# Performance work log

Measured on AMD Instinct MI355X. Metric: run time of the kernel, lower is better.

## Reference

```python
import jax, jax.numpy as jnp
import numpy as np

K = 512       # knowledge_n = node count AND feature dim
S = 50000     # student_n
E_N = 6       # exer_n (hardcoded as literal 6 in the original forward)
DEG_K = 4     # exercise neighbors per knowledge node
DEG_S = 3     # exercise neighbors per student
NEG_SLOPE = 0.2  # PyG GATConv default


def setup_inputs() -> dict:
    key = jax.random.key(0)
    ks = jax.random.split(key, 10)
    kn_emb = jax.random.normal(ks[0], (K, K), jnp.float32)
    exer_emb = jax.random.normal(ks[1], (E_N, K), jnp.float32)
    all_stu_emb = jax.random.normal(ks[2], (S, K), jnp.float32)
    # k_from_e graph: nodes = [exercises(0..5), knowledge(6..6+K-1)]
    src_ke = jax.random.randint(ks[3], (K * DEG_K,), 0, E_N)
    dst_ke = E_N + jnp.repeat(jnp.arange(K), DEG_K)
    edges_ke = jnp.stack([src_ke, dst_ke]).astype(jnp.int32)   # e -> k
    edges_ek = edges_ke[::-1]                                  # k -> e
    # u_from_e graph: nodes = [exercises(0..5), students(6..6+S-1)]
    src_ue = jax.random.randint(ks[4], (S * DEG_S,), 0, E_N)
    dst_ue = E_N + jnp.repeat(jnp.arange(S), DEG_S)
    edges_ue = jnp.stack([src_ue, dst_ue]).astype(jnp.int32)   # e -> u
    edges_eu = edges_ue[::-1]                                  # u -> e
    sc = 1.0 / np.sqrt(K)
    W_gat = jax.random.normal(ks[5], (4, K, K), jnp.float32) * sc
    a_src = jax.random.normal(ks[6], (4, K), jnp.float32) * sc
    a_dst = jax.random.normal(ks[7], (4, K), jnp.float32) * sc
    b_gat = jnp.zeros((4, K), jnp.float32)
    attn_w = jax.random.normal(ks[8], (3, 2 * K), jnp.float32) / np.sqrt(2 * K)
    attn_b = jnp.zeros((3,), jnp.float32)
    return dict(kn_emb=kn_emb, exer_emb=exer_emb, all_stu_emb=all_stu_emb,
                W_gat=W_gat, a_src=a_src, a_dst=a_dst, b_gat=b_gat,
                attn_w=attn_w, attn_b=attn_b,
                edges_ke=edges_ke, edges_ek=edges_ek,
                edges_ue=edges_ue, edges_eu=edges_eu)


def _gat(x, edges, W, a_s, a_d, b, n):
    """Single-head PyG GATConv with self-loops. edges[0]=src, edges[1]=dst."""
    h = x @ W                                   # [n, K]
    loop = jnp.arange(n, dtype=edges.dtype)
    src = jnp.concatenate([edges[0], loop])
    dst = jnp.concatenate([edges[1], loop])
    alpha_s = h @ a_s                           # [n]
    alpha_d = h @ a_d
    e = jax.nn.leaky_relu(alpha_s[src] + alpha_d[dst], NEG_SLOPE)
    emax = jax.lax.stop_gradient(jax.ops.segment_max(e, dst, num_segments=n))
    ex = jnp.exp(e - emax[dst])
    den = jax.ops.segment_sum(ex, dst, num_segments=n)
    alpha = ex / den[dst]                       # per-dst softmax
    out = jax.ops.segment_sum(alpha[:, None] * h[src], dst, num_segments=n)
    return out + b


def reference(kn_emb, exer_emb, all_stu_emb, W_gat, a_src, a_dst, b_gat,
              attn_w, attn_b, edges_ke, edges_ek, edges_ue, edges_eu):
    e_k = jnp.concatenate([exer_emb, kn_emb], axis=0)        # [6+K, K]
    e_u = jnp.concatenate([exer_emb, all_stu_emb], axis=0)   # [6+S, K]
    n_ek, n_eu = e_k.shape[0], e_u.shape[0]
    k_from_e = _gat(e_k, edges_ke, W_gat[0], a_src[0], a_dst[0], b_gat[0], n_ek)
    e_from_k = _gat(e_k, edges_ek, W_gat[1], a_src[1], a_dst[1], b_gat[1], n_ek)
    u_from_e = _gat(e_u, edges_ue, W_gat[2], a_src[2], a_dst[2], b_gat[2], n_eu)
    e_from_u = _gat(e_u, edges_eu, W_gat[3], a_src[3], a_dst[3], b_gat[3], n_eu)
    # knowledge fusion (softmax over a single column -> all ones, kept faithful)
    D = k_from_e[E_N:]
    s3 = jnp.concatenate([kn_emb, D], axis=1) @ attn_w[0] + attn_b[0]   # [K]
    sc = jax.nn.softmax(s3[:, None], axis=1)
    kn_out = kn_emb + sc[:, 0:1] * D
    # exercise fusion: 2-way attention over knowledge/student messages
    B = e_from_k[:E_N]
    C = e_from_u[:E_N]
    s1 = jnp.concatenate([exer_emb, B], axis=1) @ attn_w[1] + attn_b[1]
    s2 = jnp.concatenate([exer_emb, C], axis=1) @ attn_w[2] + attn_b[2]
    sc2 = jax.nn.softmax(jnp.stack([s1, s2], axis=1), axis=1)           # [6, 2]
    exer_out = exer_emb + sc2[:, 0:1] * B + sc2[:, 1:2] * C
    stu_out = all_stu_emb + u_from_e[E_N:]
    return (kn_out, exer_out, stu_out)
```

## Files before the change

### kernel.cpp

```cpp
#include <hip/hip_runtime.h>

typedef __attribute__((ext_vector_type(4))) float f4;
typedef __attribute__((ext_vector_type(8))) short s8;

__device__ __forceinline__ unsigned short f2bf(float x){
  unsigned u = __float_as_uint(x);
  u += 0x7fffu + ((u >> 16) & 1u);
  return (unsigned short)(u >> 16);
}
__device__ __forceinline__ float lrelu(float v){ return v > 0.f ? v : 0.2f * v; }
__device__ __forceinline__ void gload16(const unsigned short* g, unsigned short* l){
  __builtin_amdgcn_global_load_lds((const __attribute__((address_space(1))) unsigned int*)g,
                                   (__attribute__((address_space(3))) unsigned int*)l, 16, 0, 0);
}

__global__ __launch_bounds__(256) void prep(const float* __restrict__ Wg,
    const float* __restrict__ a_src, const float* __restrict__ a_dst,
    const float* __restrict__ exer, float* __restrict__ pq, float* __restrict__ zbase,
    unsigned short* __restrict__ W2T, unsigned short* __restrict__ W0T,
    float* __restrict__ HE2, float* __restrict__ HE0)
{
  __shared__ float tile[32][33];
  __shared__ float xs[512];
  const int b = blockIdx.x, t = threadIdx.x;
  if (b < 512){
    const int m = b >> 8, kb = (b & 15) * 32, nb = ((b >> 4) & 15) * 32;
    const float* W = Wg + (m == 0 ? 2 * 262144 : 0);
    unsigned short* WT = (m == 0) ? W2T : W0T;
    const int tx = t & 31, ty = t >> 5;
    #pragma unroll
    for (int i = 0; i < 32; i += 8) tile[ty + i][tx] = W[(kb + ty + i) * 512 + nb + tx];
    __syncthreads();
    #pragma unroll
    for (int i = 0; i < 32; i += 8) WT[(nb + ty + i) * 512 + kb + tx] = f2bf(tile[tx][ty + i]);
  } else if (b < 768){
    const int tid = (b - 512) * 256 + t;
    if (tid < 12304) zbase[tid] = 0.f;
    const int wid = tid >> 6, lane = tid & 63;
    for (int task = wid; task < 4096; task += 1024){
      int g = task >> 10, isq = (task >> 9) & 1, r = task & 511;
      const float* w = Wg + ((g * 512 + r) << 9);
      const float* a = (isq ? a_dst : a_src) + g * 512;
      float s = 0.f;
      for (int i = lane; i < 512; i += 64) s += w[i] * a[i];
      for (int off = 32; off; off >>= 1) s += __shfl_down(s, off);
      if (lane == 0) pq[task] = s;
    }
  } else {
    const int b3 = b - 768;
    const int g = (b3 < 6) ? 0 : 2, e = b3 % 6;
    xs[t] = exer[e * 512 + t]; xs[t + 256] = exer[e * 512 + 256 + t];
    __syncthreads();
    const float* W = Wg + g * 262144;
    float a0 = 0.f, a1 = 0.f;
    #pragma unroll 8
    for (int k = 0; k < 512; k++){ float xv = xs[k]; a0 += xv * W[k * 512 + t]; a1 += xv * W[k * 512 + 256 + t]; }
    float* HE = (g == 0) ? HE0 : HE2;
    HE[e * 512 + t] = a0; HE[e * 512 + 256 + t] = a1;
  }
}

template<int DEG>
__device__ void pass1_body(float* sC, float* sDen, float* sASE, float* sADE,
                           int bid, int nblk, const float* __restrict__ x,
                           const float* __restrict__ exer, const float* __restrict__ pq,
                           int gA, int gB, const int* __restrict__ idx,
                           float* __restrict__ alph, float* __restrict__ Craw,
                           float* __restrict__ den, int M)
{
  const int t = threadIdx.x, lane = t & 63, w = t >> 6;
  for (int i = t; i < 3072; i += 256) sC[i] = 0.f;
  if (t < 6) sDen[t] = 0.f;
  for (int d = w * 3; d < w * 3 + 3; d++){
    const float* X = exer + (d % 6) * 512;
    const float* V = (d < 6) ? (pq + gA * 1024) : (pq + gB * 1024 + 512);
    float s = 0.f;
    for (int i = lane; i < 512; i += 64) s += X[i] * V[i];
    for (int off = 32; off; off >>= 1) s += __shfl_down(s, off);
    if (lane == 0) ((d < 6) ? sASE : sADE)[d % 6] = s;
  }
  __syncthreads();

  const int kb = lane * 8;
  const float* pqA = pq + gA * 1024;
  const float* pqB = pq + gB * 1024;
  f4 pA0 = *(const f4*)(pqA + kb),       pA1 = *(const f4*)(pqA + kb + 4);
  f4 qA0 = *(const f4*)(pqA + 512 + kb), qA1 = *(const f4*)(pqA + 512 + kb + 4);
  f4 pB0 = *(const f4*)(pqB + kb),       pB1 = *(const f4*)(pqB + kb + 4);
  const float aseR = sASE[lane % 6];
  const float adeR = sADE[lane % 6];

  float cacc[6][8];
  #pragma unroll
  for (int e = 0; e < 6; e++)
    #pragma unroll
    for (int i = 0; i < 8; i++) cacc[e][i] = 0.f;
  float dacc[6] = {0.f,0.f,0.f,0.f,0.f,0.f};

  const int gw = bid * 4 + w, nw = nblk * 4;
  for (int r = gw; r < M; r += nw){
    const float* xr = x + (size_t)r * 512;
    f4 x0 = *(const f4*)(xr + kb), x1 = *(const f4*)(xr + kb + 4);
    float dP = 0.f, dQ = 0.f, dB = 0.f;
    #pragma unroll
    for (int i = 0; i < 4; i++){
      dP += x0[i]*pA0[i] + x1[i]*pA1[i];
      dQ += x0[i]*qA0[i] + x1[i]*qA1[i];
      dB += x0[i]*pB0[i] + x1[i]*pB1[i];
    }
    #pragma unroll
    for (int off = 1; off < 64; off <<= 1){
      dP += __shfl_xor(dP, off); dQ += __shfl_xor(dQ, off); dB += __shfl_xor(dB, off);
    }
    int ei[DEG];
    #pragma unroll
    for (int j = 0; j < DEG; j++) ei[j] = idx[r * DEG + j];
    float scS = lrelu(dP + dQ);
    float sc[DEG], m = scS;
    #pragma unroll
    for (int j = 0; j < DEG; j++){ sc[j] = lrelu(__shfl(aseR, ei[j]) + dQ); m = fmaxf(m, sc[j]); }
    float eS = __expf(scS - m), sum = eS;
    float ev[DEG];
    #pragma unroll
    for (int j = 0; j < DEG; j++){ ev[j] = __expf(sc[j] - m); sum += ev[j]; }
    float inv = 1.f / sum;
    float val = 0.f;
    if (lane == 0) val = eS * inv;
    else if (lane < 7){
      #pragma unroll
      for (int j = 0; j < DEG; j++) val += (ei[j] == lane - 1) ? ev[j] * inv : 0.f;
    }
    if (lane < 8) alph[(size_t)r * 8 + lane] = val;
    float wj[DEG];
    #pragma unroll
    for (int j = 0; j < DEG; j++) wj[j] = __expf(lrelu(dB + __shfl(adeR, ei[j])));
    #pragma unroll
    for (int e = 0; e < 6; e++){
      float we = 0.f;
      #pragma unroll
      for (int j = 0; j < DEG; j++) we += (ei[j] == e) ? wj[j] : 0.f;
      dacc[e] += we;
      #pragma unroll
      for (int i = 0; i < 4; i++){ cacc[e][i] += we * x0[i]; cacc[e][4+i] += we * x1[i]; }
    }
  }
  #pragma unroll
  for (int e = 0; e < 6; e++)
    #pragma unroll
    for (int i = 0; i < 8; i++)
      atomicAdd(&sC[e * 512 + kb + i], cacc[e][i]);
  if (lane == 0){
    #pragma unroll
    for (int e = 0; e < 6; e++) atomicAdd(&sDen[e], dacc[e]);
  }
  __syncthreads();
  for (int i = t; i < 3072; i += 256){
    float v = sC[i];
    if (v != 0.f) atomicAdd(&Craw[i], v);
  }
  if (t < 6) atomicAdd(&den[t], sDen[t]);
}

__global__ __launch_bounds__(256) void pass1_all(const float* __restrict__ stu,
    const float* __restrict__ kn, const float* __restrict__ exer,
    const float* __restrict__ pq, const int* __restrict__ e_ue, const int* __restrict__ e_ke,
    float* __restrict__ alphS, float* __restrict__ alphK,
    float* __restrict__ Craw3, float* __restrict__ Craw1,
    float* __restrict__ den3, float* __restrict__ den1)
{
  __shared__ float sC[3072];
  __shared__ float sDen[6], sASE[6], sADE[6];
  if (blockIdx.x < 768)
    pass1_body<3>(sC, sDen, sASE, sADE, blockIdx.x, 768, stu, exer, pq, 2, 3,
                  e_ue, alphS, Craw3, den3, 50000);
  else
    pass1_body<4>(sC, sDen, sASE, sADE, blockIdx.x - 768, 8, kn, exer, pq, 0, 1,
                  e_ke, alphK, Craw1, den1, 512);
}

__launch_bounds__(256, 3)
__global__ void gemm_all(const float* __restrict__ stu, const float* __restrict__ kn,
                         const unsigned short* __restrict__ W2T, const unsigned short* __restrict__ W0T,
                         const float* __restrict__ alphS, const float* __restrict__ alphK,
                         const float* __restrict__ HE2, const float* __restrict__ HE0,
                         const float* __restrict__ b_gat, float* __restrict__ outS,
                         float* __restrict__ outK)
{
  __shared__ __align__(16) unsigned short sA[8192];
  __shared__ __align__(16) unsigned short sB[8192];
  __shared__ __align__(16) float sAl[1024];
  __shared__ __align__(16) float sHEb[768];
  __shared__ __align__(16) float sBias[128];

  const int nwg = gridDim.x;
  const int q = nwg >> 3, rr = nwg & 7;
  const int xcd = blockIdx.x & 7, pos = blockIdx.x >> 3;
  const int wido = (xcd < rr ? xcd * (q + 1) : rr * (q + 1) + (xcd - rr) * q) + pos;

  const float* x; const unsigned short* WT; const float* alph; const float* HE;
  const float* bias; float* outp; int M, mb, nb;
  if (wido < 1564){
    x = stu; WT = W2T; alph = alphS; HE = HE2; bias = b_gat + 1024; outp = outS; M = 50000;
    mb = wido >> 2; nb = wido & 3;
  } else {
    const int w2 = wido - 1564;
    x = kn; WT = W0T; alph = alphK; HE = HE0; bias = b_gat; outp = outK; M = 512;
    mb = w2 >> 2; nb = w2 & 3;
  }
  const int r0 = mb * 128, n0 = nb * 128;
  const int tid = threadIdx.x, lane = tid & 63, w = tid >> 6;
  const int wr = w >> 1, wc = w & 1, l16 = lane & 15, lhi = lane >> 4;

  const int arow = tid >> 1, akh = (tid & 1) * 16;
  const float* aptr = x + (size_t)min(r0 + arow, M - 1) * 512 + akh;
  const int akey = (arow >> 1) & 3, s0 = (tid & 1) * 2;
  const int dA0 = arow * 32 + ((s0 ^ akey) << 3);
  const int dA1 = arow * 32 + (((s0 + 1) ^ akey) << 3);

  const int brow = tid >> 2, bslot = tid & 3;
  const int bkey = (brow >> 1) & 3;
  const unsigned short* gB0 = WT + (size_t)(n0 + brow) * 512 + ((bslot ^ bkey) << 3);
  const unsigned short* gB1 = gB0 + (size_t)64 * 512;
  unsigned short* lB0 = sB + tid * 8;
  unsigned short* lB1 = sB + 2048 + tid * 8;

  int aoff[4], boff[4];
  #pragma unroll
  for (int m = 0; m < 4; m++){
    const int ra = wr * 64 + m * 16 + l16;
    aoff[m] = ra * 32 + ((lhi ^ ((ra >> 1) & 3)) << 3);
    const int rb = wc * 64 + m * 16 + l16;
    boff[m] = rb * 32 + ((lhi ^ ((rb >> 1) & 3)) << 3);
  }

  gload16(gB0, lB0); gload16(gB1, lB1);
  f4 c0 = *(const f4*)(aptr),     c1 = *(const f4*)(aptr + 4);
  f4 c2 = *(const f4*)(aptr + 8), c3 = *(const f4*)(aptr + 12);
  {
    s8 p0, p1;
    #pragma unroll
    for (int i = 0; i < 4; i++){
      p0[i] = (short)f2bf(c0[i]); p0[4+i] = (short)f2bf(c1[i]);
      p1[i] = (short)f2bf(c2[i]); p1[4+i] = (short)f2bf(c3[i]);
    }
    *(s8*)(sA + dA0) = p0; *(s8*)(sA + dA1) = p1;
  }
  { const int rw = min(r0 + (tid >> 1), M - 1);
    *(f4*)(sAl + tid * 4) = *(const f4*)(alph + (size_t)rw * 8 + (tid & 1) * 4); }
  if (tid < 192) *(f4*)(sHEb + tid * 4) = *(const f4*)(HE + (tid >> 5) * 512 + n0 + (tid & 31) * 4);
  else if (tid < 224){ const int i2 = tid - 192; *(f4*)(sBias + i2 * 4) = *(const f4*)(bias + n0 + i2 * 4); }
  __syncthreads();

  f4 acc[4][4];
  #pragma unroll
  for (int m = 0; m < 4; m++)
    #pragma unroll
    for (int n = 0; n < 4; n++) acc[m][n] = (f4){0.f, 0.f, 0.f, 0.f};

  int bufo = 0;
  #pragma unroll 1
  for (int kt = 0; kt < 16; kt++){
    const int nxt = bufo ^ 4096;
    if (kt < 15){
      gload16(gB0 + (kt + 1) * 32, lB0 + nxt);
      gload16(gB1 + (kt + 1) * 32, lB1 + nxt);
      c0 = *(const f4*)(aptr + (kt + 1) * 32);     c1 = *(const f4*)(aptr + (kt + 1) * 32 + 4);
      c2 = *(const f4*)(aptr + (kt + 1) * 32 + 8); c3 = *(const f4*)(aptr + (kt + 1) * 32 + 12);
    }
    s8 af[4], bf[4];
    #pragma unroll
    for (int m = 0; m < 4; m++) af[m] = *(const s8*)(sA + bufo + aoff[m]);
    #pragma unroll
    for (int n = 0; n < 4; n++) bf[n] = *(const s8*)(sB + bufo + boff[n]);
    #pragma unroll
    for (int m = 0; m < 4; m++)
      #pragma unroll
      for (int n = 0; n < 4; n++)
        acc[m][n] = __builtin_amdgcn_mfma_f32_16x16x32_bf16(af[m], bf[n], acc[m][n], 0, 0, 0);
    if (kt < 15){
      s8 p0, p1;
      #pragma unroll
      for (int i = 0; i < 4; i++){
        p0[i] = (short)f2bf(c0[i]); p0[4+i] = (short)f2bf(c1[i]);
        p1[i] = (short)f2bf(c2[i]); p1[4+i] = (short)f2bf(c3[i]);
      }
      *(s8*)(sA + nxt + dA0) = p0; *(s8*)(sA + nxt + dA1) = p1;
    }
    __syncthreads();
    bufo = nxt;
  }

  float hec[4][6], bi[4];
  #pragma unroll
  for (int n = 0; n < 4; n++){
    const int cl = wc * 64 + n * 16 + l16;
    bi[n] = sBias[cl];
    #pragma unroll
    for (int e = 0; e < 6; e++) hec[n][e] = sHEb[e * 128 + cl];
  }
  #pragma unroll
  for (int m = 0; m < 4; m++){
    #pragma unroll
    for (int j = 0; j < 4; j++){
      const int rl = wr * 64 + m * 16 + lhi * 4 + j;
      const int gr = r0 + rl;
      if (gr < M){
        f4 alA = *(const f4*)(sAl + rl * 8);
        f4 alB = *(const f4*)(sAl + rl * 8 + 4);
        #pragma unroll
        for (int n = 0; n < 4; n++){
          const int gc = n0 + wc * 64 + n * 16 + l16;
          float v = x[(size_t)gr * 512 + gc] + alA[0] * acc[m][n][j] + bi[n];
          v += alA[1] * hec[n][0] + alA[2] * hec[n][1] + alA[3] * hec[n][2];
          v += alB[0] * hec[n][3] + alB[1] * hec[n][4] + alB[2] * hec[n][5];
          outp[(size_t)gr * 512 + gc] = v;
        }
      }
    }
  }
}

__global__ __launch_bounds__(512) void fin_bc(const float* __restrict__ exer,
    const float* __restrict__ Wg, const float* __restrict__ pq,
    const float* __restrict__ Craw3, const float* __restrict__ den3,
    const float* __restrict__ Craw1, const float* __restrict__ den1,
    const float* __restrict__ b_gat, float* __restrict__ B, float* __restrict__ C)
{
  const int b = blockIdx.x, ks = blockIdx.y;
  const int isC = (b >= 6) ? 1 : 0, e = b % 6, g = isC ? 3 : 1;
  const float* Craw = isC ? Craw3 : Craw1;
  const float* den  = isC ? den3  : den1;
  __shared__ float mix[64];
  __shared__ float sdots[2];
  const int t = threadIdx.x, lane = t & 63, w = t >> 6;
  if (w < 2){
    const float* V = pq + g * 1024 + w * 512;
    const float* X = exer + e * 512;
    float s = 0.f;
    for (int i = lane; i < 512; i += 64) s += X[i] * V[i];
    for (int off = 32; off; off >>= 1) s += __shfl_down(s, off);
    if (lane == 0) sdots[w] = s;
  }
  __syncthreads();
  const float wself = __expf(lrelu(sdots[0] + sdots[1]));
  const float dn = den[e] + wself;
  if (t < 64){
    const int k = ks * 64 + t;
    mix[t] = (Craw[e * 512 + k] + wself * exer[e * 512 + k]) / dn;
  }
  __syncthreads();
  const float* W = Wg + g * 262144 + ks * 64 * 512;
  float acc = 0.f;
  #pragma unroll 4
  for (int kk = 0; kk < 64; kk++) acc += mix[kk] * W[kk * 512 + t];
  if (ks == 0) acc += b_gat[g * 512 + t];
  atomicAdd(&(isC ? C : B)[e * 512 + t], acc);
}

__global__ __launch_bounds__(512) void fin_exer(const float* __restrict__ exer,
    const float* __restrict__ B, const float* __restrict__ C,
    const float* __restrict__ attn_w, const float* __restrict__ attn_b,
    float* __restrict__ outE)
{
  __shared__ float s1[6], s2[6];
  const int t = threadIdx.x, wid = t >> 6, lane = t & 63;
  for (int task = wid; task < 12; task += 8){
    int e = task >> 1, which = task & 1;
    const float* w = attn_w + (which + 1) * 1024;
    const float* X = exer + e * 512;
    const float* Y = (which ? C : B) + e * 512;
    float s = 0.f;
    for (int i = lane; i < 512; i += 64) s += X[i] * w[i] + Y[i] * w[512 + i];
    for (int off = 32; off; off >>= 1) s += __shfl_down(s, off);
    if (lane == 0) (which ? s2 : s1)[e] = s + attn_b[which + 1];
  }
  __syncthreads();
  for (int i = t; i < 3072; i += 512){
    int e = i >> 9;
    float a = s1[e], b = s2[e];
    float m = fmaxf(a, b);
    float ea = __expf(a - m), eb = __expf(b - m);
    float inv = 1.f / (ea + eb);
    outE[i] = exer[i] + (ea * inv) * B[i] + (eb * inv) * C[i];
  }
}

extern "C" void kernel_launch(void* const* d_in, const int* in_sizes, int n_in,
                              void* d_out, int out_size, void* d_ws, size_t ws_size,
                              hipStream_t stream){
  const float* kn     = (const float*)d_in[0];
  const float* exer   = (const float*)d_in[1];
  const float* stu    = (const float*)d_in[2];
  const float* Wg     = (const float*)d_in[3];
  const float* a_src  = (const float*)d_in[4];
  const float* a_dst  = (const float*)d_in[5];
  const float* b_gat  = (const float*)d_in[6];
  const float* attn_w = (const float*)d_in[7];
  const float* attn_b = (const float*)d_in[8];
  const int*   e_ke   = (const int*)d_in[9];
  const int*   e_ue   = (const int*)d_in[11];
  float* out = (float*)d_out;

  unsigned short* W2T = (unsigned short*)d_ws;
  unsigned short* W0T = W2T + 262144;
  float* pq    = (float*)(W0T + 262144);
  float* Craw3 = pq + 4096;
  float* Craw1 = Craw3 + 3072;
  float* den3  = Craw1 + 3072;
  float* den1  = den3 + 8;
  float* Bb    = den1 + 8;
  float* Cc    = Bb + 3072;
  float* HE2   = Cc + 3072;
  float* HE0   = HE2 + 3072;
  float* alphS = HE0 + 3072;
  float* alphK = alphS + 400384;

  hipLaunchKernelGGL(prep, dim3(780), dim3(256), 0, stream,
                     Wg, a_src, a_dst, exer, pq, Craw3, W2T, W0T, HE2, HE0);
  hipLaunchKernelGGL(pass1_all, dim3(776), dim3(256), 0, stream,
                     stu, kn, exer, pq, e_ue, e_ke, alphS, alphK, Craw3, Craw1, den3, den1);
  hipLaunchKernelGGL(gemm_all, dim3(1580), dim3(256), 0, stream,
                     stu, kn, W2T, W0T, alphS, alphK, HE2, HE0, b_gat, out + 265216, out);
  hipLaunchKernelGGL(fin_bc, dim3(12, 8), dim3(512), 0, stream,
                     exer, Wg, pq, Craw3, den3, Craw1, den1, b_gat, Bb, Cc);
  hipLaunchKernelGGL(fin_exer, dim3(1), dim3(512), 0, stream,
                     exer, Bb, Cc, attn_w, attn_b, out + 262144);
}
```

Before: 403.2 us.

## Prefetch next row in pass1, double grid, and split atomics into eight partial slices

Pass1 now software-pipelines its row loop, loading the next row's features and edge indices before computing the current row, to hide global load latency. The student grid is roughly doubled to raise occupancy. Global atomic accumulation of the exercise sums and denominators is spread over eight partial slices, selected by block index, to reduce atomic contention. fin_bc then sums those slices, and prep zeroes the larger partial buffers. The cost is extra registers for the prefetched data, more workspace, and a few more loads in fin_bc.

New measurement: 427.2 us. +5.9%, slower.

```diff
diff --git a/kernel.cpp b/kernel.cpp
--- a/kernel.cpp
+++ b/kernel.cpp
@@ -35,7 +35,7 @@
     for (int i = 0; i < 32; i += 8) WT[(nb + ty + i) * 512 + kb + tx] = f2bf(tile[tx][ty + i]);
   } else if (b < 768){
     const int tid = (b - 512) * 256 + t;
-    if (tid < 12304) zbase[tid] = 0.f;
+    if (tid < 55424) zbase[tid] = 0.f;
     const int wid = tid >> 6, lane = tid & 63;
     for (int task = wid; task < 4096; task += 1024){
       int g = task >> 10, isq = (task >> 9) & 1, r = task & 511;
@@ -65,8 +65,8 @@
                            int bid, int nblk, const float* __restrict__ x,
                            const float* __restrict__ exer, const float* __restrict__ pq,
                            int gA, int gB, const int* __restrict__ idx,
-                           float* __restrict__ alph, float* __restrict__ Craw,
-                           float* __restrict__ den, int M)
+                           float* __restrict__ alph, float* __restrict__ CrawP,
+                           float* __restrict__ denP, int M)
 {
   const int t = threadIdx.x, lane = t & 63, w = t >> 6;
   for (int i = t; i < 3072; i += 256) sC[i] = 0.f;
@@ -97,51 +97,66 @@
     for (int i = 0; i < 8; i++) cacc[e][i] = 0.f;
   float dacc[6] = {0.f,0.f,0.f,0.f,0.f,0.f};
 
-  const int gw = bid * 4 + w, nw = nblk * 4;
-  for (int r = gw; r < M; r += nw){
-    const float* xr = x + (size_t)r * 512;
-    f4 x0 = *(const f4*)(xr + kb), x1 = *(const f4*)(xr + kb + 4);
-    float dP = 0.f, dQ = 0.f, dB = 0.f;
-    #pragma unroll
-    for (int i = 0; i < 4; i++){
-      dP += x0[i]*pA0[i] + x1[i]*pA1[i];
-      dQ += x0[i]*qA0[i] + x1[i]*qA1[i];
-      dB += x0[i]*pB0[i] + x1[i]*pB1[i];
-    }
-    #pragma unroll
-    for (int off = 1; off < 64; off <<= 1){
-      dP += __shfl_xor(dP, off); dQ += __shfl_xor(dQ, off); dB += __shfl_xor(dB, off);
-    }
+  const int nw = nblk * 4;
+  int r = bid * 4 + w;
+  if (r < M){
+    const float* xr = x + (size_t)r * 512 + kb;
+    f4 x0 = *(const f4*)(xr), x1 = *(const f4*)(xr + 4);
     int ei[DEG];
     #pragma unroll
     for (int j = 0; j < DEG; j++) ei[j] = idx[r * DEG + j];
-    float scS = lrelu(dP + dQ);
-    float sc[DEG], m = scS;
-    #pragma unroll
-    for (int j = 0; j < DEG; j++){ sc[j] = lrelu(__shfl(aseR, ei[j]) + dQ); m = fmaxf(m, sc[j]); }
-    float eS = __expf(scS - m), sum = eS;
-    float ev[DEG];
-    #pragma unroll
-    for (int j = 0; j < DEG; j++){ ev[j] = __expf(sc[j] - m); sum += ev[j]; }
-    float inv = 1.f / sum;
-    float val = 0.f;
-    if (lane == 0) val = eS * inv;
-    else if (lane < 7){
-      #pragma unroll
-      for (int j = 0; j < DEG; j++) val += (ei[j] == lane - 1) ? ev[j] * inv : 0.f;
-    }
-    if (lane < 8) alph[(size_t)r * 8 + lane] = val;
-    float wj[DEG];
-    #pragma unroll
-    for (int j = 0; j < DEG; j++) wj[j] = __expf(lrelu(dB + __shfl(adeR, ei[j])));
-    #pragma unroll
-    for (int e = 0; e < 6; e++){
-      float we = 0.f;
-      #pragma unroll
-      for (int j = 0; j < DEG; j++) we += (ei[j] == e) ? wj[j] : 0.f;
-      dacc[e] += we;
-      #pragma unroll
-      for (int i = 0; i < 4; i++){ cacc[e][i] += we * x0[i]; cacc[e][4+i] += we * x1[i]; }
+    while (true){
+      const int rn = r + nw;
+      f4 y0, y1; int ein[DEG];
+      if (rn < M){
+        const float* xn = x + (size_t)rn * 512 + kb;
+        y0 = *(const f4*)(xn); y1 = *(const f4*)(xn + 4);
+        #pragma unroll
+        for (int j = 0; j < DEG; j++) ein[j] = idx[rn * DEG + j];
+      }
+      float dP = 0.f, dQ = 0.f, dB = 0.f;
+      #pragma unroll
+      for (int i = 0; i < 4; i++){
+        dP += x0[i]*pA0[i] + x1[i]*pA1[i];
+        dQ += x0[i]*qA0[i] + x1[i]*qA1[i];
+        dB += x0[i]*pB0[i] + x1[i]*pB1[i];
+      }
+      #pragma unroll
+      for (int off = 1; off < 64; off <<= 1){
+        dP += __shfl_xor(dP, off); dQ += __shfl_xor(dQ, off); dB += __shfl_xor(dB, off);
+      }
+      float scS = lrelu(dP + dQ);
+      float sc[DEG], m = scS;
+      #pragma unroll
+      for (int j = 0; j < DEG; j++){ sc[j] = lrelu(__shfl(aseR, ei[j]) + dQ); m = fmaxf(m, sc[j]); }
+      float eS = __expf(scS - m), sum = eS;
+      float ev[DEG];
+      #pragma unroll
+      for (int j = 0; j < DEG; j++){ ev[j] = __expf(sc[j] - m); sum += ev[j]; }
+      float inv = 1.f / sum;
+      float val = 0.f;
+      if (lane == 0) val = eS * inv;
+      else if (lane < 7){
+        #pragma unroll
+        for (int j = 0; j < DEG; j++) val += (ei[j] == lane - 1) ? ev[j] * inv : 0.f;
+      }
+      if (lane < 8) alph[(size_t)r * 8 + lane] = val;
+      float wj[DEG];
+      #pragma unroll
+      for (int j = 0; j < DEG; j++) wj[j] = __expf(lrelu(dB + __shfl(adeR, ei[j])));
+      #pragma unroll
+      for (int e = 0; e < 6; e++){
+        float we = 0.f;
+        #pragma unroll
+        for (int j = 0; j < DEG; j++) we += (ei[j] == e) ? wj[j] : 0.f;
+        dacc[e] += we;
+        #pragma unroll
+        for (int i = 0; i < 4; i++){ cacc[e][i] += we * x0[i]; cacc[e][4+i] += we * x1[i]; }
+      }
+      if (rn >= M) break;
+      r = rn; x0 = y0; x1 = y1;
+      #pragma unroll
+      for (int j = 0; j < DEG; j++) ei[j] = ein[j];
     }
   }
   #pragma unroll
@@ -154,28 +169,29 @@
     for (int e = 0; e < 6; e++) atomicAdd(&sDen[e], dacc[e]);
   }
   __syncthreads();
+  float* Cslice = CrawP + (bid & 7) * 3072;
   for (int i = t; i < 3072; i += 256){
     float v = sC[i];
-    if (v != 0.f) atomicAdd(&Craw[i], v);
-  }
-  if (t < 6) atomicAdd(&den[t], sDen[t]);
+    if (v != 0.f) atomicAdd(&Cslice[i], v);
+  }
+  if (t < 6) atomicAdd(&denP[(bid & 7) * 8 + t], sDen[t]);
 }
 
 __global__ __launch_bounds__(256) void pass1_all(const float* __restrict__ stu,
     const float* __restrict__ kn, const float* __restrict__ exer,
     const float* __restrict__ pq, const int* __restrict__ e_ue, const int* __restrict__ e_ke,
     float* __restrict__ alphS, float* __restrict__ alphK,
-    float* __restrict__ Craw3, float* __restrict__ Craw1,
-    float* __restrict__ den3, float* __restrict__ den1)
+    float* __restrict__ CrawP3, float* __restrict__ CrawP1,
+    float* __restrict__ denP3, float* __restrict__ denP1)
 {
   __shared__ float sC[3072];
   __shared__ float sDen[6], sASE[6], sADE[6];
-  if (blockIdx.x < 768)
-    pass1_body<3>(sC, sDen, sASE, sADE, blockIdx.x, 768, stu, exer, pq, 2, 3,
-                  e_ue, alphS, Craw3, den3, 50000);
+  if (blockIdx.x < 1528)
+    pass1_body<3>(sC, sDen, sASE, sADE, blockIdx.x, 1528, stu, exer, pq, 2, 3,
+                  e_ue, alphS, CrawP3, denP3, 50000);
   else
-    pass1_body<4>(sC, sDen, sASE, sADE, blockIdx.x - 768, 8, kn, exer, pq, 0, 1,
-                  e_ke, alphK, Craw1, den1, 512);
+    pass1_body<4>(sC, sDen, sASE, sADE, blockIdx.x - 1528, 8, kn, exer, pq, 0, 1,
+                  e_ke, alphK, CrawP1, denP1, 512);
 }
 
 __launch_bounds__(256, 3)
@@ -322,14 +338,14 @@
 
 __global__ __launch_bounds__(512) void fin_bc(const float* __restrict__ exer,
     const float* __restrict__ Wg, const float* __restrict__ pq,
-    const float* __restrict__ Craw3, const float* __restrict__ den3,
-    const float* __restrict__ Craw1, const float* __restrict__ den1,
+    const float* __restrict__ CrawP3, const float* __restrict__ denP3,
+    const float* __restrict__ CrawP1, const float* __restrict__ denP1,
     const float* __restrict__ b_gat, float* __restrict__ B, float* __restrict__ C)
 {
   const int b = blockIdx.x, ks = blockIdx.y;
   const int isC = (b >= 6) ? 1 : 0, e = b % 6, g = isC ? 3 : 1;
-  const float* Craw = isC ? Craw3 : Craw1;
-  const float* den  = isC ? den3  : den1;
+  const float* CrawP = isC ? CrawP3 : CrawP1;
+  const float* denP  = isC ? denP3  : denP1;
   __shared__ float mix[64];
   __shared__ float sdots[2];
   const int t = threadIdx.x, lane = t & 63, w = t >> 6;
@@ -343,10 +359,15 @@
   }
   __syncthreads();
   const float wself = __expf(lrelu(sdots[0] + sdots[1]));
-  const float dn = den[e] + wself;
+  float dn = wself;
+  #pragma unroll
+  for (int s = 0; s < 8; s++) dn += denP[s * 8 + e];
   if (t < 64){
     const int k = ks * 64 + t;
-    mix[t] = (Craw[e * 512 + k] + wself * exer[e * 512 + k]) / dn;
+    float cr = 0.f;
+    #pragma unroll
+    for (int s = 0; s < 8; s++) cr += CrawP[s * 3072 + e * 512 + k];
+    mix[t] = (cr + wself * exer[e * 512 + k]) / dn;
   }
   __syncthreads();
   const float* W = Wg + g * 262144 + ks * 64 * 512;
@@ -403,26 +424,26 @@
 
   unsigned short* W2T = (unsigned short*)d_ws;
   unsigned short* W0T = W2T + 262144;
-  float* pq    = (float*)(W0T + 262144);
-  float* Craw3 = pq + 4096;
-  float* Craw1 = Craw3 + 3072;
-  float* den3  = Craw1 + 3072;
-  float* den1  = den3 + 8;
-  float* Bb    = den1 + 8;
-  float* Cc    = Bb + 3072;
-  float* HE2   = Cc + 3072;
-  float* HE0   = HE2 + 3072;
-  float* alphS = HE0 + 3072;
-  float* alphK = alphS + 400384;
+  float* pq     = (float*)(W0T + 262144);
+  float* CrawP3 = pq + 4096;
+  float* CrawP1 = CrawP3 + 24576;
+  float* denP3  = CrawP1 + 24576;
+  float* denP1  = denP3 + 64;
+  float* Bb     = denP1 + 64;
+  float* Cc     = Bb + 3072;
+  float* HE2    = Cc + 3072;
+  float* HE0    = HE2 + 3072;
+  float* alphS  = HE0 + 3072;
+  float* alphK  = alphS + 400384;
 
   hipLaunchKernelGGL(prep, dim3(780), dim3(256), 0, stream,
-                     Wg, a_src, a_dst, exer, pq, Craw3, W2T, W0T, HE2, HE0);
-  hipLaunchKernelGGL(pass1_all, dim3(776), dim3(256), 0, stream,
-                     stu, kn, exer, pq, e_ue, e_ke, alphS, alphK, Craw3, Craw1, den3, den1);
+                     Wg, a_src, a_dst, exer, pq, CrawP3, W2T, W0T, HE2, HE0);
+  hipLaunchKernelGGL(pass1_all, dim3(1536), dim3(256), 0, stream,
+                     stu, kn, exer, pq, e_ue, e_ke, alphS, alphK, CrawP3, CrawP1, denP3, denP1);
   hipLaunchKernelGGL(gemm_all, dim3(1580), dim3(256), 0, stream,
                      stu, kn, W2T, W0T, alphS, alphK, HE2, HE0, b_gat, out + 265216, out);
   hipLaunchKernelGGL(fin_bc, dim3(12, 8), dim3(512), 0, stream,
-                     exer, Wg, pq, Craw3, den3, Craw1, den1, b_gat, Bb, Cc);
+                     exer, Wg, pq, CrawP3, denP3, CrawP1, denP1, b_gat, Bb, Cc);
   hipLaunchKernelGGL(fin_exer, dim3(1), dim3(512), 0, stream,
                      exer, Bb, Cc, attn_w, attn_b, out + 262144);
 }
```
